# Optimization experiments

Hardware: AMD Instinct MI355X
Metric: run time of the kernel (lower is better)

Reference implementation:

```python
import jax, jax.numpy as jnp
import numpy as np

E, K = 8, 2  # num_experts, top_k


def setup_inputs() -> dict:
    key = jax.random.key(0)
    ks = jax.random.split(key, 5)
    B, S, H, I = 2, 1024, 1024, 4096
    scale_h = 1.0 / np.sqrt(H)
    scale_i = 1.0 / np.sqrt(I)
    return {
        "hidden_states": jax.random.normal(ks[0], (B, S, H), jnp.float32),
        "conf_w": jax.random.normal(ks[1], (E, H), jnp.float32) * 0.1 * scale_h,
        "conf_b": jnp.zeros((E,), jnp.float32),
        "gate_w": jax.random.normal(ks[2], (E, I, H), jnp.float32) * scale_h,
        "up_w": jax.random.normal(ks[3], (E, I, H), jnp.float32) * scale_h,
        "down_w": jax.random.normal(ks[4], (E, H, I), jnp.float32) * scale_i,
        "wealth": jnp.ones((E,), jnp.float32),
    }


def reference(hidden_states, conf_w, conf_b, gate_w, up_w, down_w, wealth):
    x = hidden_states  # (B,S,H)
    # Per-expert confidence heads: sigmoid(Linear(H->1)) stacked -> (B,S,E)
    confidences = jax.nn.sigmoid(jnp.einsum("bsh,eh->bse", x, conf_w) + conf_b)
    # VCG auction: bid = confidence * wealth
    bids = confidences * wealth  # (B,S,E)
    top_bids, selected_experts = jax.lax.top_k(bids, K)  # (B,S,K)
    # payments = (K+1)-th highest bid (unused in output but part of forward math)
    sorted_bids = -jnp.sort(-bids, axis=-1)
    payments = jnp.broadcast_to(sorted_bids[..., K:K + 1], top_bids.shape)
    routing_weights = jax.nn.softmax(top_bids, axis=-1)  # (B,S,K)
    # combine weights per expert: sum_k rw_k * [sel_k == e] -> (B,S,E)
    combine = jnp.sum(
        jax.nn.one_hot(selected_experts, E, dtype=x.dtype)
        * routing_weights[..., None],
        axis=2,
    )

    def ffn(gw, uw, dw):
        # SwiGLU expert: down(silu(gate(x)) * up(x))
        g = jnp.einsum("bsh,ih->bsi", x, gw)
        u = jnp.einsum("bsh,ih->bsi", x, uw)
        return jnp.einsum("bsi,hi->bsh", jax.nn.silu(g) * u, dw)

    expert_out = jax.vmap(ffn)(gate_w, up_w, down_w)  # (E,B,S,H)
    output = jnp.einsum("ebsh,bse->bsh", expert_out, combine)
    return output
```

## Files before the change

kernel.cpp:

```cpp
#include <hip/hip_runtime.h>
#include <math.h>

#define NEXP 8
#define TILE 128
#define BK 32

typedef __attribute__((ext_vector_type(8))) short short8;
typedef __attribute__((ext_vector_type(4))) float float4v;

__device__ __forceinline__ unsigned short f2bf(float f) {
  union { float f; unsigned u; } v; v.f = f;
  unsigned r = v.u + 0x7FFFu + ((v.u >> 16) & 1u);
  return (unsigned short)(r >> 16);
}
__device__ __forceinline__ unsigned pack2(float a, float b) {
  return (unsigned)f2bf(a) | ((unsigned)f2bf(b) << 16);
}

__device__ __forceinline__ void gll16(const void* g, void* l) {
  __builtin_amdgcn_global_load_lds(
      (const __attribute__((address_space(1))) unsigned int*)(unsigned long long)(uintptr_t)g,
      (__attribute__((address_space(3))) unsigned int*)(unsigned)(uintptr_t)l,
      16, 0, 0);
}

__global__ __launch_bounds__(256) void convert_x_kernel(
    const float* __restrict__ x, unsigned short* __restrict__ xb, int n4) {
  int i = blockIdx.x * 256 + threadIdx.x;
  if (i >= n4) return;
  float4 v = ((const float4*)x)[i];
  uint2 o; o.x = pack2(v.x, v.y); o.y = pack2(v.z, v.w);
  ((uint2*)xb)[i] = o;
}

__global__ __launch_bounds__(256) void pack_w_kernel(
    const float* __restrict__ src, unsigned short* __restrict__ dst, int K) {
  const int ks = blockIdx.x, rt = blockIdx.y, e = blockIdx.z;
  const int n_ks = gridDim.x, n_rt = gridDim.y;
  const int r = threadIdx.x >> 1, half = threadIdx.x & 1;
  const size_t R = (size_t)n_rt * TILE;
  const float4* s = (const float4*)(src + ((size_t)e * R + rt * TILE + r) * K + ks * BK + half * 16);
  float4 v0 = s[0], v1 = s[1], v2 = s[2], v3 = s[3];
  uint4 o0, o1;
  o0.x = pack2(v0.x, v0.y); o0.y = pack2(v0.z, v0.w);
  o0.z = pack2(v1.x, v1.y); o0.w = pack2(v1.z, v1.w);
  o1.x = pack2(v2.x, v2.y); o1.y = pack2(v2.z, v2.w);
  o1.z = pack2(v3.x, v3.y); o1.w = pack2(v3.z, v3.w);
  unsigned short* pb = dst + ((size_t)(e * n_rt + rt) * n_ks + ks) * (TILE * BK)
                           + (r >> 4) * 512 + (r & 15) * 8;
  *(uint4*)(pb + (2 * half) * 128)     = o0;
  *(uint4*)(pb + (2 * half + 1) * 128) = o1;
}

__global__ __launch_bounds__(256) void routing_kernel(
    const float* __restrict__ x, const float* __restrict__ cw,
    const float* __restrict__ cb, const float* __restrict__ wealth,
    int* __restrict__ plist, int* __restrict__ counts,
    float* __restrict__ w_rt, int T, int H) {
  const int t = blockIdx.x;
  const int tid = threadIdx.x;
  const float* xr = x + (size_t)t * H;
  float acc[NEXP];
#pragma unroll
  for (int e = 0; e < NEXP; ++e) acc[e] = 0.f;
  for (int h = tid; h < H; h += 256) {
    float xv = xr[h];
#pragma unroll
    for (int e = 0; e < NEXP; ++e) acc[e] += xv * cw[e * H + h];
  }
  __shared__ float s[NEXP][256];
#pragma unroll
  for (int e = 0; e < NEXP; ++e) s[e][tid] = acc[e];
  __syncthreads();
  for (int st = 128; st > 0; st >>= 1) {
    if (tid < st) {
#pragma unroll
      for (int e = 0; e < NEXP; ++e) s[e][tid] += s[e][tid + st];
    }
    __syncthreads();
  }
  if (tid == 0) {
    float bids[NEXP];
#pragma unroll
    for (int e = 0; e < NEXP; ++e) {
      float lg = s[e][0] + cb[e];
      float c = 1.f / (1.f + expf(-lg));
      bids[e] = c * wealth[e];
    }
    int i0 = 0;
    for (int e = 1; e < NEXP; ++e) if (bids[e] > bids[i0]) i0 = e;
    int i1 = (i0 == 0) ? 1 : 0;
    for (int e = 0; e < NEXP; ++e) if (e != i0 && bids[e] > bids[i1]) i1 = e;
    float ex = expf(bids[i1] - bids[i0]);
    float wsum = 1.f + ex;
    w_rt[2 * t]     = 1.f / wsum;
    w_rt[2 * t + 1] = ex / wsum;
    int p0 = atomicAdd(&counts[i0], 1);
    plist[i0 * T + p0] = 2 * t;
    int p1 = atomicAdd(&counts[i1], 1);
    plist[i1 * T + p1] = 2 * t + 1;
  }
}

__global__ __launch_bounds__(256, 2) void gateup_kernel(
    const unsigned short* __restrict__ xb, const unsigned short* __restrict__ gwp,
    const unsigned short* __restrict__ uwp, const int* __restrict__ plist,
    const int* __restrict__ counts, unsigned short* __restrict__ act,
    int T, int H, int I) {
  const int nx = gridDim.x, ny = gridDim.y, nz = gridDim.z;
  int rt = blockIdx.x, it = blockIdx.y, e = blockIdx.z;
  {
    int nwg = nx * ny * nz;
    if (((nwg & 7) == 0) && (((nwg >> 3) % nx) == 0)) {
      int orig = blockIdx.x + nx * (blockIdx.y + ny * blockIdx.z);
      int idx = orig >> 3, xcd = orig & 7;
      int q = idx / nx;
      rt = idx - q * nx;
      int chunk = q * 8 + xcd;
      it = chunk % ny;
      e = chunk / ny;
    }
  }
  const int cnt = counts[e];
  const int row0 = rt * TILE;
  if (row0 >= cnt) return;
  const int nks = H / BK;

  __shared__ __align__(16) unsigned short As[2][TILE * BK];
  __shared__ __align__(16) unsigned short Bg[2][TILE * BK];
  __shared__ __align__(16) unsigned short Bu[2][TILE * BK];

  const int tid = threadIdx.x, lane = tid & 63, wv = tid >> 6;
  const int wm = wv >> 1, wn = wv & 1;
  const int quad = lane >> 4, l15 = lane & 15;

  int ri0 = row0 + wv * 32 + l15;
  int ri1 = ri0 + 16;
  if (ri0 >= cnt) ri0 = cnt - 1;
  if (ri1 >= cnt) ri1 = cnt - 1;
  const unsigned short* a0 = xb + (size_t)(plist[e * T + ri0] >> 1) * H + quad * 8;
  const unsigned short* a1 = xb + (size_t)(plist[e * T + ri1] >> 1) * H + quad * 8;

  const size_t pan = ((size_t)(e * ny + it) * nks) * (TILE * BK);
  const unsigned short* g0 = gwp + pan + (size_t)wv * 1024 + (size_t)lane * 8;
  const unsigned short* u0 = uwp + pan + (size_t)wv * 1024 + (size_t)lane * 8;

  float4v accg[4][4], accu[4][4];
#pragma unroll
  for (int a = 0; a < 4; ++a)
#pragma unroll
    for (int b = 0; b < 4; ++b) {
      float4v z = {0.f, 0.f, 0.f, 0.f};
      accg[a][b] = z; accu[a][b] = z;
    }

  auto stage = [&](int kk, int b) {
    unsigned short* lA = &As[b][wv * 1024];
    unsigned short* lG = &Bg[b][wv * 1024];
    unsigned short* lU = &Bu[b][wv * 1024];
    size_t ka = (size_t)kk * BK;
    size_t kb = (size_t)kk * (TILE * BK);
    gll16(a0 + ka, lA);       gll16(a1 + ka, lA + 512);
    gll16(g0 + kb, lG);       gll16(g0 + kb + 512, lG + 512);
    gll16(u0 + kb, lU);       gll16(u0 + kb + 512, lU + 512);
  };

  stage(0, 0);
  __syncthreads();
  for (int k = 0; k < nks; ++k) {
    const int cb = k & 1;
    if (k + 1 < nks) stage(k + 1, cb ^ 1);
    short8 af[4], bgf[4], buf_[4];
#pragma unroll
    for (int mi = 0; mi < 4; ++mi)
      af[mi] = *(const short8*)(&As[cb][(wm * 4 + mi) * 512 + quad * 128 + l15 * 8]);
#pragma unroll
    for (int ni = 0; ni < 4; ++ni) {
      bgf[ni]  = *(const short8*)(&Bg[cb][(wn * 4 + ni) * 512 + quad * 128 + l15 * 8]);
      buf_[ni] = *(const short8*)(&Bu[cb][(wn * 4 + ni) * 512 + quad * 128 + l15 * 8]);
    }
#pragma unroll
    for (int mi = 0; mi < 4; ++mi)
#pragma unroll
      for (int ni = 0; ni < 4; ++ni) {
        accg[mi][ni] = __builtin_amdgcn_mfma_f32_16x16x32_bf16(af[mi], bgf[ni], accg[mi][ni], 0, 0, 0);
        accu[mi][ni] = __builtin_amdgcn_mfma_f32_16x16x32_bf16(af[mi], buf_[ni], accu[mi][ni], 0, 0, 0);
      }
    __syncthreads();
  }

#pragma unroll
  for (int mi = 0; mi < 4; ++mi) {
    int rbase = wm * 64 + mi * 16 + quad * 4;
#pragma unroll
    for (int r = 0; r < 4; ++r) {
      int grow = row0 + rbase + r;
      if (grow < cnt) {
        int p = plist[e * T + grow];
        size_t base = (size_t)p * I + it * TILE + wn * 64 + l15;
#pragma unroll
        for (int ni = 0; ni < 4; ++ni) {
          float g = accg[mi][ni][r];
          float u = accu[mi][ni][r];
          float s = g / (1.f + __expf(-g)) * u;
          act[base + ni * 16] = f2bf(s);
        }
      }
    }
  }
}

__global__ __launch_bounds__(256, 2) void down_kernel(
    const unsigned short* __restrict__ act, const unsigned short* __restrict__ dwp,
    const int* __restrict__ plist, const int* __restrict__ counts,
    float* __restrict__ part, int T, int H, int I) {
  const int nx = gridDim.x, ny = gridDim.y, nz = gridDim.z;
  int rt = blockIdx.x, ht = blockIdx.y, zz = blockIdx.z;
  {
    int nwg = nx * ny * nz;
    if (((nwg & 7) == 0) && (((nwg >> 3) % nx) == 0)) {
      int orig = blockIdx.x + nx * (blockIdx.y + ny * blockIdx.z);
      int idx = orig >> 3, xcd = orig & 7;
      int q = idx / nx;
      rt = idx - q * nx;
      int chunk = q * 8 + xcd;
      ht = chunk % ny;
      zz = chunk / ny;
    }
  }
  const int e = zz >> 1, split = zz & 1;
  const int cnt = counts[e];
  const int row0 = rt * TILE;
  if (row0 >= cnt) return;
  const int nks_tot = I / BK;
  const int nks = nks_tot >> 1;
  const int k0 = split * nks;

  __shared__ __align__(16) unsigned short As[2][TILE * BK];
  __shared__ __align__(16) unsigned short Bs[2][TILE * BK];

  const int tid = threadIdx.x, lane = tid & 63, wv = tid >> 6;
  const int wm = wv >> 1, wn = wv & 1;
  const int quad = lane >> 4, l15 = lane & 15;

  int ri0 = row0 + wv * 32 + l15;
  int ri1 = ri0 + 16;
  if (ri0 >= cnt) ri0 = cnt - 1;
  if (ri1 >= cnt) ri1 = cnt - 1;
  const unsigned short* a0 = act + (size_t)plist[e * T + ri0] * I + k0 * BK + quad * 8;
  const unsigned short* a1 = act + (size_t)plist[e * T + ri1] * I + k0 * BK + quad * 8;

  const size_t pan = ((size_t)(e * ny + ht) * nks_tot + k0) * (TILE * BK);
  const unsigned short* b0 = dwp + pan + (size_t)wv * 1024 + (size_t)lane * 8;

  float4v acc[4][4];
#pragma unroll
  for (int a = 0; a < 4; ++a)
#pragma unroll
    for (int b = 0; b < 4; ++b) { float4v z = {0.f, 0.f, 0.f, 0.f}; acc[a][b] = z; }

  auto stage = [&](int kk, int b) {
    unsigned short* lA = &As[b][wv * 1024];
    unsigned short* lB = &Bs[b][wv * 1024];
    size_t ka = (size_t)kk * BK;
    size_t kb = (size_t)kk * (TILE * BK);
    gll16(a0 + ka, lA);  gll16(a1 + ka, lA + 512);
    gll16(b0 + kb, lB);  gll16(b0 + kb + 512, lB + 512);
  };

  stage(0, 0);
  __syncthreads();
  for (int k = 0; k < nks; ++k) {
    const int cb = k & 1;
    if (k + 1 < nks) stage(k + 1, cb ^ 1);
    short8 af[4], bf[4];
#pragma unroll
    for (int mi = 0; mi < 4; ++mi)
      af[mi] = *(const short8*)(&As[cb][(wm * 4 + mi) * 512 + quad * 128 + l15 * 8]);
#pragma unroll
    for (int ni = 0; ni < 4; ++ni)
      bf[ni] = *(const short8*)(&Bs[cb][(wn * 4 + ni) * 512 + quad * 128 + l15 * 8]);
#pragma unroll
    for (int mi = 0; mi < 4; ++mi)
#pragma unroll
      for (int ni = 0; ni < 4; ++ni)
        acc[mi][ni] = __builtin_amdgcn_mfma_f32_16x16x32_bf16(af[mi], bf[ni], acc[mi][ni], 0, 0, 0);
    __syncthreads();
  }

#pragma unroll
  for (int mi = 0; mi < 4; ++mi) {
    int rbase = wm * 64 + mi * 16 + quad * 4;
#pragma unroll
    for (int r = 0; r < 4; ++r) {
      int grow = row0 + rbase + r;
      if (grow < cnt) {
        int p = plist[e * T + grow];
        size_t base = ((size_t)split * 2 * T + p) * H + ht * TILE + wn * 64 + l15;
#pragma unroll
        for (int ni = 0; ni < 4; ++ni)
          part[base + ni * 16] = acc[mi][ni][r];
      }
    }
  }
}

__global__ __launch_bounds__(256) void combine_kernel(
    const float* __restrict__ part, const float* __restrict__ w_rt,
    float* __restrict__ out, int T, int H) {
  int h4 = H >> 2;
  int n4 = T * h4;
  int i = blockIdx.x * 256 + threadIdx.x;
  if (i >= n4) return;
  int t = i / h4;
  int c = i - t * h4;
  float w0 = w_rt[2 * t], w1 = w_rt[2 * t + 1];
  size_t splitoff = (size_t)2 * T * H / 4;
  const float4* pa = (const float4*)(part + (size_t)(2 * t) * H);
  const float4* pb = (const float4*)(part + (size_t)(2 * t + 1) * H);
  float4 a0 = pa[c], a1 = pa[c + splitoff];
  float4 b0 = pb[c], b1 = pb[c + splitoff];
  float4 o;
  o.x = w0 * (a0.x + a1.x) + w1 * (b0.x + b1.x);
  o.y = w0 * (a0.y + a1.y) + w1 * (b0.y + b1.y);
  o.z = w0 * (a0.z + a1.z) + w1 * (b0.z + b1.z);
  o.w = w0 * (a0.w + a1.w) + w1 * (b0.w + b1.w);
  ((float4*)(out + (size_t)t * H))[c] = o;
}

extern "C" void kernel_launch(void* const* d_in, const int* in_sizes, int n_in,
                              void* d_out, int out_size, void* d_ws, size_t ws_size,
                              hipStream_t stream) {
  const float* x      = (const float*)d_in[0];
  const float* cw     = (const float*)d_in[1];
  const float* cb     = (const float*)d_in[2];
  const float* gw     = (const float*)d_in[3];
  const float* uw     = (const float*)d_in[4];
  const float* dw     = (const float*)d_in[5];
  const float* wealth = (const float*)d_in[6];
  float* out = (float*)d_out;

  const int H = in_sizes[1] / NEXP;
  const int T = in_sizes[0] / H;
  const int I = in_sizes[3] / (NEXP * H);

  char* ws = (char*)d_ws;
  size_t off = 0;
  unsigned short* xb  = (unsigned short*)(ws + off); off += (size_t)T * H * 2;
  unsigned short* act = (unsigned short*)(ws + off); off += (size_t)2 * T * I * 2;
  float* part = (float*)(ws + off); off += (size_t)2 * 2 * T * H * 4;
  unsigned short* gwp = (unsigned short*)(ws + off); off += (size_t)NEXP * I * H * 2;
  unsigned short* uwp = (unsigned short*)(ws + off); off += (size_t)NEXP * I * H * 2;
  unsigned short* dwp = gwp;
  int* plist = (int*)(ws + off); off += (size_t)NEXP * T * 4;
  float* w_rt = (float*)(ws + off); off += (size_t)T * 2 * 4;
  int* counts = (int*)(ws + off); off += NEXP * 4;

  hipMemsetAsync(counts, 0, NEXP * sizeof(int), stream);

  int n4 = (T * H) / 4;
  convert_x_kernel<<<(n4 + 255) / 256, 256, 0, stream>>>(x, xb, n4);
  routing_kernel<<<T, 256, 0, stream>>>(x, cw, cb, wealth, plist, counts, w_rt, T, H);

  dim3 gp(H / BK, I / TILE, NEXP);
  pack_w_kernel<<<gp, 256, 0, stream>>>(gw, gwp, H);
  pack_w_kernel<<<gp, 256, 0, stream>>>(uw, uwp, H);

  int ttiles = (T + TILE - 1) / TILE;
  dim3 g1(ttiles, I / TILE, NEXP);
  gateup_kernel<<<g1, 256, 0, stream>>>(xb, gwp, uwp, plist, counts, act, T, H, I);

  dim3 gpd(I / BK, H / TILE, NEXP);
  pack_w_kernel<<<gpd, 256, 0, stream>>>(dw, dwp, I);

  dim3 g2(ttiles, H / TILE, NEXP * 2);
  down_kernel<<<g2, 256, 0, stream>>>(act, dwp, plist, counts, part, T, H, I);

  combine_kernel<<<(n4 + 255) / 256, 256, 0, stream>>>(part, w_rt, out, T, H);
}
```

Measured before the change: 692.6 us.

## Fuse prep kernels and deepen GEMM pipeline with direct A loads

Merges x conversion, routing and gate/up weight packing into one launch, and routing now uses one wavefront per token with shuffle reductions. The gate/up and down GEMMs load A fragments straight from global memory into registers (double-buffered) and keep only B in LDS with a 4-stage ring. Explicit vmcnt waits plus barriers replace __syncthreads. The down kernel raises its occupancy hint to 3. This cuts launch overhead and LDS traffic and hides more latency, but relies on hand-tuned waitcnt values and uncoalesced per-row A loads.

```diff
diff --git a/kernel.cpp b/kernel.cpp
--- a/kernel.cpp
+++ b/kernel.cpp
@@ -22,15 +22,6 @@
       (const __attribute__((address_space(1))) unsigned int*)(unsigned long long)(uintptr_t)g,
       (__attribute__((address_space(3))) unsigned int*)(unsigned)(uintptr_t)l,
       16, 0, 0);
-}
-
-__global__ __launch_bounds__(256) void convert_x_kernel(
-    const float* __restrict__ x, unsigned short* __restrict__ xb, int n4) {
-  int i = blockIdx.x * 256 + threadIdx.x;
-  if (i >= n4) return;
-  float4 v = ((const float4*)x)[i];
-  uint2 o; o.x = pack2(v.x, v.y); o.y = pack2(v.z, v.w);
-  ((uint2*)xb)[i] = o;
 }
 
 __global__ __launch_bounds__(256) void pack_w_kernel(
@@ -52,55 +43,98 @@
   *(uint4*)(pb + (2 * half + 1) * 128) = o1;
 }
 
-__global__ __launch_bounds__(256) void routing_kernel(
+__global__ __launch_bounds__(256) void prep_kernel(
+    const float* __restrict__ gw, const float* __restrict__ uw,
     const float* __restrict__ x, const float* __restrict__ cw,
     const float* __restrict__ cb, const float* __restrict__ wealth,
-    int* __restrict__ plist, int* __restrict__ counts,
-    float* __restrict__ w_rt, int T, int H) {
-  const int t = blockIdx.x;
-  const int tid = threadIdx.x;
-  const float* xr = x + (size_t)t * H;
-  float acc[NEXP];
-#pragma unroll
-  for (int e = 0; e < NEXP; ++e) acc[e] = 0.f;
-  for (int h = tid; h < H; h += 256) {
-    float xv = xr[h];
-#pragma unroll
-    for (int e = 0; e < NEXP; ++e) acc[e] += xv * cw[e * H + h];
-  }
-  __shared__ float s[NEXP][256];
-#pragma unroll
-  for (int e = 0; e < NEXP; ++e) s[e][tid] = acc[e];
-  __syncthreads();
-  for (int st = 128; st > 0; st >>= 1) {
-    if (tid < st) {
-#pragma unroll
-      for (int e = 0; e < NEXP; ++e) s[e][tid] += s[e][tid + st];
-    }
-    __syncthreads();
-  }
-  if (tid == 0) {
-    float bids[NEXP];
+    unsigned short* __restrict__ gwp, unsigned short* __restrict__ uwp,
+    unsigned short* __restrict__ xb, int* __restrict__ plist,
+    int* __restrict__ counts, float* __restrict__ w_rt,
+    int T, int H, int n4, int z_conv, int z_rout) {
+  const int z = blockIdx.z;
+  if (z < z_conv) {
+    const int e = (z < NEXP) ? z : z - NEXP;
+    const float* src = (z < NEXP) ? gw : uw;
+    unsigned short* dst = (z < NEXP) ? gwp : uwp;
+    const int ks = blockIdx.x, rt = blockIdx.y;
+    const int n_ks = gridDim.x, n_rt = gridDim.y;
+    const int r = threadIdx.x >> 1, half = threadIdx.x & 1;
+    const int K = H;
+    const size_t R = (size_t)n_rt * TILE;
+    const float4* s = (const float4*)(src + ((size_t)e * R + rt * TILE + r) * K + ks * BK + half * 16);
+    float4 v0 = s[0], v1 = s[1], v2 = s[2], v3 = s[3];
+    uint4 o0, o1;
+    o0.x = pack2(v0.x, v0.y); o0.y = pack2(v0.z, v0.w);
+    o0.z = pack2(v1.x, v1.y); o0.w = pack2(v1.z, v1.w);
+    o1.x = pack2(v2.x, v2.y); o1.y = pack2(v2.z, v2.w);
+    o1.z = pack2(v3.x, v3.y); o1.w = pack2(v3.z, v3.w);
+    unsigned short* pb = dst + ((size_t)(e * n_rt + rt) * n_ks + ks) * (TILE * BK)
+                             + (r >> 4) * 512 + (r & 15) * 8;
+    *(uint4*)(pb + (2 * half) * 128)     = o0;
+    *(uint4*)(pb + (2 * half + 1) * 128) = o1;
+  } else if (z < z_rout) {
+    int bl = blockIdx.y * gridDim.x + blockIdx.x;
+    int i = ((z - z_conv) * gridDim.x * gridDim.y + bl) * 256 + threadIdx.x;
+    if (i < n4) {
+      float4 v = ((const float4*)x)[i];
+      uint2 o; o.x = pack2(v.x, v.y); o.y = pack2(v.z, v.w);
+      ((uint2*)xb)[i] = o;
+    }
+  } else {
+    int bl = blockIdx.y * gridDim.x + blockIdx.x;
+    int t = ((z - z_rout) * gridDim.x * gridDim.y + bl) * 4 + (threadIdx.x >> 6);
+    if (t >= T) return;
+    const int lane = threadIdx.x & 63;
+    const float4* x4 = (const float4*)(x + (size_t)t * H);
+    const float4* c4 = (const float4*)cw;
+    const int h4n = H >> 2;
+    float acc[NEXP];
+#pragma unroll
+    for (int e = 0; e < NEXP; ++e) acc[e] = 0.f;
+    for (int h = lane; h < h4n; h += 64) {
+      float4 xv = x4[h];
+#pragma unroll
+      for (int e = 0; e < NEXP; ++e) {
+        float4 cv = c4[(size_t)e * h4n + h];
+        acc[e] += xv.x * cv.x + xv.y * cv.y + xv.z * cv.z + xv.w * cv.w;
+      }
+    }
 #pragma unroll
     for (int e = 0; e < NEXP; ++e) {
-      float lg = s[e][0] + cb[e];
-      float c = 1.f / (1.f + expf(-lg));
-      bids[e] = c * wealth[e];
-    }
-    int i0 = 0;
-    for (int e = 1; e < NEXP; ++e) if (bids[e] > bids[i0]) i0 = e;
-    int i1 = (i0 == 0) ? 1 : 0;
-    for (int e = 0; e < NEXP; ++e) if (e != i0 && bids[e] > bids[i1]) i1 = e;
-    float ex = expf(bids[i1] - bids[i0]);
-    float wsum = 1.f + ex;
-    w_rt[2 * t]     = 1.f / wsum;
-    w_rt[2 * t + 1] = ex / wsum;
-    int p0 = atomicAdd(&counts[i0], 1);
-    plist[i0 * T + p0] = 2 * t;
-    int p1 = atomicAdd(&counts[i1], 1);
-    plist[i1 * T + p1] = 2 * t + 1;
-  }
-}
+      float v = acc[e];
+#pragma unroll
+      for (int off = 32; off > 0; off >>= 1) v += __shfl_down(v, off, 64);
+      acc[e] = v;
+    }
+    if (lane == 0) {
+      float bids[NEXP];
+#pragma unroll
+      for (int e = 0; e < NEXP; ++e) {
+        float lg = acc[e] + cb[e];
+        float c = 1.f / (1.f + expf(-lg));
+        bids[e] = c * wealth[e];
+      }
+      int i0 = 0;
+      for (int e = 1; e < NEXP; ++e) if (bids[e] > bids[i0]) i0 = e;
+      int i1 = (i0 == 0) ? 1 : 0;
+      for (int e = 0; e < NEXP; ++e) if (e != i0 && bids[e] > bids[i1]) i1 = e;
+      float ex = expf(bids[i1] - bids[i0]);
+      float wsum = 1.f + ex;
+      w_rt[2 * t]     = 1.f / wsum;
+      w_rt[2 * t + 1] = ex / wsum;
+      int p0 = atomicAdd(&counts[i0], 1);
+      plist[i0 * T + p0] = 2 * t;
+      int p1 = atomicAdd(&counts[i1], 1);
+      plist[i1 * T + p1] = 2 * t + 1;
+    }
+  }
+}
+
+#define GATE(N) do {                                          \
+    asm volatile("s_waitcnt vmcnt(" #N ")" ::: "memory");     \
+    __builtin_amdgcn_s_barrier();                             \
+    __builtin_amdgcn_sched_barrier(0);                        \
+  } while (0)
 
 __global__ __launch_bounds__(256, 2) void gateup_kernel(
     const unsigned short* __restrict__ xb, const unsigned short* __restrict__ gwp,
@@ -126,20 +160,20 @@
   if (row0 >= cnt) return;
   const int nks = H / BK;
 
-  __shared__ __align__(16) unsigned short As[2][TILE * BK];
-  __shared__ __align__(16) unsigned short Bg[2][TILE * BK];
-  __shared__ __align__(16) unsigned short Bu[2][TILE * BK];
+  __shared__ __align__(16) unsigned short Bg[4][TILE * BK];
+  __shared__ __align__(16) unsigned short Bu[4][TILE * BK];
 
   const int tid = threadIdx.x, lane = tid & 63, wv = tid >> 6;
   const int wm = wv >> 1, wn = wv & 1;
   const int quad = lane >> 4, l15 = lane & 15;
 
-  int ri0 = row0 + wv * 32 + l15;
-  int ri1 = ri0 + 16;
-  if (ri0 >= cnt) ri0 = cnt - 1;
-  if (ri1 >= cnt) ri1 = cnt - 1;
-  const unsigned short* a0 = xb + (size_t)(plist[e * T + ri0] >> 1) * H + quad * 8;
-  const unsigned short* a1 = xb + (size_t)(plist[e * T + ri1] >> 1) * H + quad * 8;
+  const unsigned short* ap[4];
+#pragma unroll
+  for (int mi = 0; mi < 4; ++mi) {
+    int r = row0 + wm * 64 + mi * 16 + l15;
+    if (r >= cnt) r = cnt - 1;
+    ap[mi] = xb + (size_t)(plist[e * T + r] >> 1) * H + quad * 8;
+  }
 
   const size_t pan = ((size_t)(e * ny + it) * nks) * (TILE * BK);
   const unsigned short* g0 = gwp + pan + (size_t)wv * 1024 + (size_t)lane * 8;
@@ -154,26 +188,33 @@
       accg[a][b] = z; accu[a][b] = z;
     }
 
-  auto stage = [&](int kk, int b) {
-    unsigned short* lA = &As[b][wv * 1024];
+  auto stageB = [&](int kk, int b) {
     unsigned short* lG = &Bg[b][wv * 1024];
     unsigned short* lU = &Bu[b][wv * 1024];
-    size_t ka = (size_t)kk * BK;
     size_t kb = (size_t)kk * (TILE * BK);
-    gll16(a0 + ka, lA);       gll16(a1 + ka, lA + 512);
-    gll16(g0 + kb, lG);       gll16(g0 + kb + 512, lG + 512);
-    gll16(u0 + kb, lU);       gll16(u0 + kb + 512, lU + 512);
+    gll16(g0 + kb, lG); gll16(g0 + kb + 512, lG + 512);
+    gll16(u0 + kb, lU); gll16(u0 + kb + 512, lU + 512);
   };
 
-  stage(0, 0);
-  __syncthreads();
-  for (int k = 0; k < nks; ++k) {
-    const int cb = k & 1;
-    if (k + 1 < nks) stage(k + 1, cb ^ 1);
-    short8 af[4], bgf[4], buf_[4];
+  short8 afA[4], afB[4];
+#pragma unroll
+  for (int mi = 0; mi < 4; ++mi) afA[mi] = *(const short8*)(ap[mi]);
+  __builtin_amdgcn_sched_barrier(0);
+  stageB(0, 0); stageB(1, 1); stageB(2, 2);
+  __builtin_amdgcn_sched_barrier(0);
+  GATE(8);
+
+  auto phase = [&](int k, short8 (&cur)[4], short8 (&nxt)[4]) {
+    const int cb = k & 3;
+    int ks_ = k + 3; if (ks_ >= nks) ks_ = nks - 1;
+    stageB(ks_, (k + 3) & 3);
+    __builtin_amdgcn_sched_barrier(0);
+    int ka = k + 1; if (ka >= nks) ka = nks - 1;
 #pragma unroll
     for (int mi = 0; mi < 4; ++mi)
-      af[mi] = *(const short8*)(&As[cb][(wm * 4 + mi) * 512 + quad * 128 + l15 * 8]);
+      nxt[mi] = *(const short8*)(ap[mi] + (size_t)ka * BK);
+    __builtin_amdgcn_sched_barrier(0);
+    short8 bgf[4], buf_[4];
 #pragma unroll
     for (int ni = 0; ni < 4; ++ni) {
       bgf[ni]  = *(const short8*)(&Bg[cb][(wn * 4 + ni) * 512 + quad * 128 + l15 * 8]);
@@ -183,11 +224,12 @@
     for (int mi = 0; mi < 4; ++mi)
 #pragma unroll
       for (int ni = 0; ni < 4; ++ni) {
-        accg[mi][ni] = __builtin_amdgcn_mfma_f32_16x16x32_bf16(af[mi], bgf[ni], accg[mi][ni], 0, 0, 0);
-        accu[mi][ni] = __builtin_amdgcn_mfma_f32_16x16x32_bf16(af[mi], buf_[ni], accu[mi][ni], 0, 0, 0);
+        accg[mi][ni] = __builtin_amdgcn_mfma_f32_16x16x32_bf16(cur[mi], bgf[ni], accg[mi][ni], 0, 0, 0);
+        accu[mi][ni] = __builtin_amdgcn_mfma_f32_16x16x32_bf16(cur[mi], buf_[ni], accu[mi][ni], 0, 0, 0);
       }
-    __syncthreads();
-  }
+    GATE(8);
+  };
+  for (int k = 0; k < nks; k += 2) { phase(k, afA, afB); phase(k + 1, afB, afA); }
 
 #pragma unroll
   for (int mi = 0; mi < 4; ++mi) {
@@ -210,7 +252,7 @@
   }
 }
 
-__global__ __launch_bounds__(256, 2) void down_kernel(
+__global__ __launch_bounds__(256, 3) void down_kernel(
     const unsigned short* __restrict__ act, const unsigned short* __restrict__ dwp,
     const int* __restrict__ plist, const int* __restrict__ counts,
     float* __restrict__ part, int T, int H, int I) {
@@ -236,19 +278,19 @@
   const int nks = nks_tot >> 1;
   const int k0 = split * nks;
 
-  __shared__ __align__(16) unsigned short As[2][TILE * BK];
-  __shared__ __align__(16) unsigned short Bs[2][TILE * BK];
+  __shared__ __align__(16) unsigned short Bs[4][TILE * BK];
 
   const int tid = threadIdx.x, lane = tid & 63, wv = tid >> 6;
   const int wm = wv >> 1, wn = wv & 1;
   const int quad = lane >> 4, l15 = lane & 15;
 
-  int ri0 = row0 + wv * 32 + l15;
-  int ri1 = ri0 + 16;
-  if (ri0 >= cnt) ri0 = cnt - 1;
-  if (ri1 >= cnt) ri1 = cnt - 1;
-  const unsigned short* a0 = act + (size_t)plist[e * T + ri0] * I + k0 * BK + quad * 8;
-  const unsigned short* a1 = act + (size_t)plist[e * T + ri1] * I + k0 * BK + quad * 8;
+  const unsigned short* ap[4];
+#pragma unroll
+  for (int mi = 0; mi < 4; ++mi) {
+    int r = row0 + wm * 64 + mi * 16 + l15;
+    if (r >= cnt) r = cnt - 1;
+    ap[mi] = act + (size_t)plist[e * T + r] * I + k0 * BK + quad * 8;
+  }
 
   const size_t pan = ((size_t)(e * ny + ht) * nks_tot + k0) * (TILE * BK);
   const unsigned short* b0 = dwp + pan + (size_t)wv * 1024 + (size_t)lane * 8;
@@ -259,24 +301,31 @@
 #pragma unroll
     for (int b = 0; b < 4; ++b) { float4v z = {0.f, 0.f, 0.f, 0.f}; acc[a][b] = z; }
 
-  auto stage = [&](int kk, int b) {
-    unsigned short* lA = &As[b][wv * 1024];
+  auto stageB = [&](int kk, int b) {
     unsigned short* lB = &Bs[b][wv * 1024];
-    size_t ka = (size_t)kk * BK;
     size_t kb = (size_t)kk * (TILE * BK);
-    gll16(a0 + ka, lA);  gll16(a1 + ka, lA + 512);
     gll16(b0 + kb, lB);  gll16(b0 + kb + 512, lB + 512);
   };
 
-  stage(0, 0);
-  __syncthreads();
-  for (int k = 0; k < nks; ++k) {
-    const int cb = k & 1;
-    if (k + 1 < nks) stage(k + 1, cb ^ 1);
-    short8 af[4], bf[4];
+  short8 afA[4], afB[4];
+#pragma unroll
+  for (int mi = 0; mi < 4; ++mi) afA[mi] = *(const short8*)(ap[mi]);
+  __builtin_amdgcn_sched_barrier(0);
+  stageB(0, 0); stageB(1, 1); stageB(2, 2);
+  __builtin_amdgcn_sched_barrier(0);
+  GATE(4);
+
+  auto phase = [&](int k, short8 (&cur)[4], short8 (&nxt)[4]) {
+    const int cb = k & 3;
+    int ks_ = k + 3; if (ks_ >= nks) ks_ = nks - 1;
+    stageB(ks_, (k + 3) & 3);
+    __builtin_amdgcn_sched_barrier(0);
+    int ka = k + 1; if (ka >= nks) ka = nks - 1;
 #pragma unroll
     for (int mi = 0; mi < 4; ++mi)
-      af[mi] = *(const short8*)(&As[cb][(wm * 4 + mi) * 512 + quad * 128 + l15 * 8]);
+      nxt[mi] = *(const short8*)(ap[mi] + (size_t)ka * BK);
+    __builtin_amdgcn_sched_barrier(0);
+    short8 bf[4];
 #pragma unroll
     for (int ni = 0; ni < 4; ++ni)
       bf[ni] = *(const short8*)(&Bs[cb][(wn * 4 + ni) * 512 + quad * 128 + l15 * 8]);
@@ -284,9 +333,10 @@
     for (int mi = 0; mi < 4; ++mi)
 #pragma unroll
       for (int ni = 0; ni < 4; ++ni)
-        acc[mi][ni] = __builtin_amdgcn_mfma_f32_16x16x32_bf16(af[mi], bf[ni], acc[mi][ni], 0, 0, 0);
-    __syncthreads();
-  }
+        acc[mi][ni] = __builtin_amdgcn_mfma_f32_16x16x32_bf16(cur[mi], bf[ni], acc[mi][ni], 0, 0, 0);
+    GATE(6);
+  };
+  for (int k = 0; k < nks; k += 2) { phase(k, afA, afB); phase(k + 1, afB, afA); }
 
 #pragma unroll
   for (int mi = 0; mi < 4; ++mi) {
@@ -359,12 +409,14 @@
   hipMemsetAsync(counts, 0, NEXP * sizeof(int), stream);
 
   int n4 = (T * H) / 4;
-  convert_x_kernel<<<(n4 + 255) / 256, 256, 0, stream>>>(x, xb, n4);
-  routing_kernel<<<T, 256, 0, stream>>>(x, cw, cb, wealth, plist, counts, w_rt, T, H);
-
-  dim3 gp(H / BK, I / TILE, NEXP);
-  pack_w_kernel<<<gp, 256, 0, stream>>>(gw, gwp, H);
-  pack_w_kernel<<<gp, 256, 0, stream>>>(uw, uwp, H);
+  int bps = (H / BK) * (I / TILE);
+  int nconv = (n4 + bps * 256 - 1) / (bps * 256);
+  int nrout = ((T + 3) / 4 + bps - 1) / bps;
+  int z_conv = 2 * NEXP, z_rout = z_conv + nconv;
+  dim3 gprep(H / BK, I / TILE, z_rout + nrout);
+  prep_kernel<<<gprep, 256, 0, stream>>>(gw, uw, x, cw, cb, wealth,
+                                         gwp, uwp, xb, plist, counts, w_rt,
+                                         T, H, n4, z_conv, z_rout);
 
   int ttiles = (T + TILE - 1) / TILE;
   dim3 g1(ttiles, I / TILE, NEXP);
```

Result: no change. 701.3 us (+1.3%).
